# Optimization experiments

Measured on AMD Instinct MI355X. Metric: run time of the kernel, lower is better.

Reference implementation:

```python
import jax, jax.numpy as jnp
import numpy as np

N_HEADS = 16

def setup_inputs() -> dict:
    key = jax.random.key(0)
    ks = jax.random.split(key, 5)
    D = 1024
    B, T = 4, 1024
    scale = 1.0 / np.sqrt(D)
    x = jax.random.normal(ks[0], (B, T, D), dtype=jnp.float32)
    Wq = jax.random.normal(ks[1], (D, D), dtype=jnp.float32) * scale
    Wk = jax.random.normal(ks[2], (D, D), dtype=jnp.float32) * scale
    Wv = jax.random.normal(ks[3], (D, D), dtype=jnp.float32) * scale
    Wo = jax.random.normal(ks[4], (D, D), dtype=jnp.float32) * scale
    return {"x": x, "Wq": Wq, "Wk": Wk, "Wv": Wv, "Wo": Wo}


def reference(x, Wq, Wk, Wv, Wo):
    # FLA BasedLinearAttention (mode='chunk', normalize=True, scale=1) with
    # Taylor feature map phi(u) = [1, u/d^{1/4}, (u (x) u)/sqrt(2 d)], so
    # phi(q)·phi(k) = 1 + s + s^2/2 where s = (q·k)/sqrt(d).
    B, T, D = x.shape
    H = N_HEADS
    d = D // H  # head_dim == feature_dim
    # torch Linear: y = x @ W.T (bias=False in FLA proj layers)
    q = (x @ Wq.T).reshape(B, T, H, d).transpose(0, 2, 1, 3)  # b h t d
    k = (x @ Wk.T).reshape(B, T, H, d).transpose(0, 2, 1, 3)
    v = (x @ Wv.T).reshape(B, T, H, d).transpose(0, 2, 1, 3)
    s = jnp.einsum('bhtd,bhsd->bhts', q, k) / jnp.sqrt(jnp.float32(d))
    scores = 1.0 + s + 0.5 * s * s  # always > 0 (= ((s+1)^2+1)/2)
    causal = jnp.tril(jnp.ones((T, T), dtype=bool))
    scores = jnp.where(causal, scores, 0.0)
    num = jnp.einsum('bhts,bhsd->bhtd', scores, v)
    den = jnp.sum(scores, axis=-1, keepdims=True)
    o = num / den  # b h t d
    o = o.transpose(0, 2, 1, 3).reshape(B, T, D)  # b t (h d)
    return o @ Wo.T
```

## Files before the change

### kernel.cpp

```cpp
#include <hip/hip_runtime.h>

typedef unsigned short u16;
typedef __attribute__((ext_vector_type(8))) short bf16x8;
typedef __attribute__((ext_vector_type(8))) unsigned short u16x8;
typedef __attribute__((ext_vector_type(4))) float f32x4;

#define MFMA16(a, b, c) __builtin_amdgcn_mfma_f32_16x16x32_bf16((a), (b), (c), 0, 0, 0)

__device__ __forceinline__ void gll16(const void* g, void* l) {
    __builtin_amdgcn_global_load_lds(
        (const __attribute__((address_space(1))) unsigned int*)g,
        (__attribute__((address_space(3))) unsigned int*)l, 16, 0, 0);
}

__device__ __forceinline__ u16 f2b(float f) {
    unsigned int u = __float_as_uint(f);
    u += 0x7fffu + ((u >> 16) & 1u);
    return (u16)(u >> 16);
}

__device__ __forceinline__ unsigned int pkcvt(float a, float b) {
    unsigned int r;
    asm("v_cvt_pk_bf16_f32 %0, %1, %2" : "=v"(r) : "v"(a), "v"(b));
    return r;
}

__global__ __launch_bounds__(256) void cast_all(const float* __restrict__ x,
                                                const float* __restrict__ w0,
                                                const float* __restrict__ w1,
                                                const float* __restrict__ w2,
                                                const float* __restrict__ w3,
                                                u16* __restrict__ xb,
                                                u16* __restrict__ wb) {
    const int bid = blockIdx.x;
    const float* s; u16* d; int off;
    if (bid < 2048) { s = x; d = xb; off = bid; }
    else {
        const int wi = (bid - 2048) >> 9;
        s = (wi == 0) ? w0 : (wi == 1) ? w1 : (wi == 2) ? w2 : w3;
        d = wb + (size_t)wi * 1048576;
        off = (bid - 2048) & 511;
    }
    const int i = (off * 256 + threadIdx.x) * 8;
    float4 a = *(const float4*)(s + i);
    float4 b = *(const float4*)(s + i + 4);
    *(uint4*)(d + i) = make_uint4(pkcvt(a.x, a.y), pkcvt(a.z, a.w),
                                  pkcvt(b.x, b.y), pkcvt(b.z, b.w));
}

template <int BM, int BN, int MODE, int SLOTS>
__global__ __launch_bounds__(256) void gemm_bt(const u16* __restrict__ A,
                                               const u16* __restrict__ W,
                                               void* __restrict__ Yv,
                                               u16* __restrict__ vT,
                                               int K, int ldY) {
    constexpr int MI = BM / 32, NJ = BN / 32;
    constexpr int ACH = BM / 16;
    constexpr int NPW = (BM + BN) / 64;
    __shared__ u16 As[2][SLOTS][BM * 32];
    __shared__ u16 Bs[2][SLOTS][BN * 32];
    const int t = threadIdx.x, w = t >> 6, lane = t & 63;
    const int quad = lane >> 4, m16 = lane & 15;
    const int wr = (w >> 1) * (BM / 2), wc = (w & 1) * (BN / 2);
    const int row0 = blockIdx.x * BM, col0 = blockIdx.y * BN;
    const int srow = lane >> 2, scol = (lane & 3) * 8;

    auto stage = [&](int buf, int slot, int k0) {
#pragma unroll
        for (int cc = 0; cc < NPW; ++cc) {
            const int c = w * NPW + cc;
            if (c < ACH)
                gll16(A + (size_t)(row0 + c * 16 + srow) * K + k0 + scol,
                      &As[buf][slot][c * 512]);
            else
                gll16(W + (size_t)(col0 + (c - ACH) * 16 + srow) * K + k0 + scol,
                      &Bs[buf][slot][(c - ACH) * 512]);
        }
    };

    f32x4 acc[MI][NJ];
#pragma unroll
    for (int i = 0; i < MI; ++i)
#pragma unroll
        for (int j = 0; j < NJ; ++j) acc[i][j] = (f32x4){0.f, 0.f, 0.f, 0.f};

    auto compute_tile = [&](int buf, int slot) {
        bf16x8 af[MI], bf[NJ];
#pragma unroll
        for (int i = 0; i < MI; ++i)
            af[i] = *(const bf16x8*)&As[buf][slot][(wr + i * 16 + m16) * 32 + quad * 8];
#pragma unroll
        for (int j = 0; j < NJ; ++j)
            bf[j] = *(const bf16x8*)&Bs[buf][slot][(wc + j * 16 + m16) * 32 + quad * 8];
#pragma unroll
        for (int i = 0; i < MI; ++i)
#pragma unroll
            for (int j = 0; j < NJ; ++j) acc[i][j] = MFMA16(af[i], bf[j], acc[i][j]);
    };

#pragma unroll
    for (int s = 0; s < SLOTS; ++s) stage(0, s, s * 32);
    const int ngroups = K / (32 * SLOTS);
    for (int g = 0; g < ngroups; ++g) {
        const int buf = g & 1;
        __syncthreads();
        const int kn = (g + 1) * SLOTS * 32;
        if (kn < K) {
#pragma unroll
            for (int s = 0; s < SLOTS; ++s) stage(buf ^ 1, s, kn + s * 32);
        }
#pragma unroll
        for (int s = 0; s < SLOTS; ++s) compute_tile(buf, s);
    }
    if constexpr (MODE == 0) {
#pragma unroll
        for (int i = 0; i < MI; ++i)
#pragma unroll
            for (int j = 0; j < NJ; ++j)
#pragma unroll
                for (int r = 0; r < 4; ++r)
                    ((float*)Yv)[(size_t)(row0 + wr + i * 16 + quad * 4 + r) * ldY +
                                 col0 + wc + j * 16 + m16] = acc[i][j][r];
    } else {
        if (col0 < 2048) {
            u16* qk = (u16*)Yv;
#pragma unroll
            for (int i = 0; i < MI; ++i)
#pragma unroll
                for (int j = 0; j < NJ; ++j)
#pragma unroll
                    for (int r = 0; r < 4; ++r)
                        qk[(size_t)(row0 + wr + i * 16 + quad * 4 + r) * 2048 +
                           col0 + wc + j * 16 + m16] = f2b(acc[i][j][r]);
        } else {
#pragma unroll
            for (int i = 0; i < MI; ++i) {
                const int rbase = row0 + wr + i * 16;
                const int bb = rbase >> 10;
                const int tok0 = (rbase & 1023) + quad * 4;
#pragma unroll
                for (int j = 0; j < NJ; ++j) {
                    const int vTrow = bb * 1024 + (col0 + wc + j * 16 + m16 - 2048);
                    *(uint2*)(vT + (size_t)vTrow * 1024 + tok0) =
                        make_uint2(pkcvt(acc[i][j][0], acc[i][j][1]),
                                   pkcvt(acc[i][j][2], acc[i][j][3]));
                }
            }
        }
    }
}

__global__ __launch_bounds__(256) void based_attn(const u16* __restrict__ qkm,
                                                  const u16* __restrict__ vT,
                                                  u16* __restrict__ o) {
    __shared__ u16 ks[2][2][2][64][32];
    __shared__ u16 vs[2][2][2][64][32];
    __shared__ u16 SsA[2][64][32];
    __shared__ u16 SsB[2][64][32];

    const int t = threadIdx.x, w = t >> 6, lane = t & 63;
    const int quad = lane >> 4, m16 = lane & 15;
    const int p = blockIdx.x, h = blockIdx.y, b = blockIdx.z;
    const int tA = p, tB = 15 - p;
    const int srow = lane >> 2, s8 = (lane & 3) * 8;
    const int qrow = w * 16 + m16;

    const size_t qbase = (size_t)b * 1024 * 2048 + h * 64;
    const size_t kbase = qbase + 1024;
    const size_t vbase = ((size_t)b * 1024 + h * 64) * 1024;

    bf16x8 qfA[2], qfB[2];
#pragma unroll
    for (int kd = 0; kd < 2; ++kd) {
        qfA[kd] = *(const bf16x8*)(qkm + qbase +
                   (size_t)(tA * 64 + qrow) * 2048 + kd * 32 + quad * 8);
        qfB[kd] = *(const bf16x8*)(qkm + qbase +
                   (size_t)(tB * 64 + qrow) * 2048 + kd * 32 + quad * 8);
    }

    auto stage_tile = [&](int kt, int buf, int slot) {
#pragma unroll
        for (int cc = 0; cc < 2; ++cc) {
            const int c = w * 2 + cc;
            const int blk = c >> 2, rc = c & 3;
            gll16(qkm + kbase + (size_t)(kt * 64 + rc * 16 + srow) * 2048 + blk * 32 + s8,
                  &ks[buf][slot][blk][rc * 16][0]);
            gll16(vT + vbase + (size_t)(rc * 16 + srow) * 1024 + kt * 64 + blk * 32 + s8,
                  &vs[buf][slot][blk][rc * 16][0]);
        }
    };

    bf16x8 ones;
#pragma unroll
    for (int e = 0; e < 8; ++e) ones[e] = (short)0x3F80;

    f32x4 numA[4], numB[4], denA, denB;
    denA = denB = (f32x4){0.f, 0.f, 0.f, 0.f};
#pragma unroll
    for (int j = 0; j < 4; ++j) numA[j] = numB[j] = (f32x4){0.f, 0.f, 0.f, 0.f};

    auto compute = [&](int buf, int slot, int kt) {
        const bool doA = (kt <= tA);
        f32x4 sA[4], sB[4];
#pragma unroll
        for (int jk = 0; jk < 4; ++jk)
            sA[jk] = sB[jk] = (f32x4){0.f, 0.f, 0.f, 0.f};
        __builtin_amdgcn_s_setprio(1);
#pragma unroll
        for (int kd = 0; kd < 2; ++kd)
#pragma unroll
            for (int jk = 0; jk < 4; ++jk) {
                bf16x8 af = *(const bf16x8*)&ks[buf][slot][kd][jk * 16 + m16][quad * 8];
                sB[jk] = MFMA16(af, qfB[kd], sB[jk]);
                if (doA) sA[jk] = MFMA16(af, qfA[kd], sA[jk]);
            }
        __builtin_amdgcn_s_setprio(0);
#pragma unroll
        for (int jk = 0; jk < 4; ++jk) {
            const int kl = jk * 16 + quad * 4;
            float scB[4];
#pragma unroll
            for (int r = 0; r < 4; ++r) {
                const float u = fmaf(sB[jk][r], 0.125f, 1.0f);
                scB[r] = fmaf(u * 0.5f, u, 0.5f);
            }
            if (kt == tB) {
#pragma unroll
                for (int r = 0; r < 4; ++r)
                    if (kl + r > qrow) scB[r] = 0.f;
            }
            *(uint2*)&SsB[kl >> 5][qrow][kl & 31] =
                make_uint2(pkcvt(scB[0], scB[1]), pkcvt(scB[2], scB[3]));
            if (doA) {
                float scA[4];
#pragma unroll
                for (int r = 0; r < 4; ++r) {
                    const float u = fmaf(sA[jk][r], 0.125f, 1.0f);
                    scA[r] = fmaf(u * 0.5f, u, 0.5f);
                }
                if (kt == tA) {
#pragma unroll
                    for (int r = 0; r < 4; ++r)
                        if (kl + r > qrow) scA[r] = 0.f;
                }
                *(uint2*)&SsA[kl >> 5][qrow][kl & 31] =
                    make_uint2(pkcvt(scA[0], scA[1]), pkcvt(scA[2], scA[3]));
            }
        }
        __builtin_amdgcn_s_setprio(1);
#pragma unroll
        for (int kb = 0; kb < 2; ++kb) {
            bf16x8 vf[4];
#pragma unroll
            for (int j = 0; j < 4; ++j)
                vf[j] = *(const bf16x8*)&vs[buf][slot][kb][j * 16 + m16][quad * 8];
            bf16x8 sfB = *(const bf16x8*)&SsB[kb][qrow][quad * 8];
#pragma unroll
            for (int j = 0; j < 4; ++j) numB[j] = MFMA16(sfB, vf[j], numB[j]);
            denB = MFMA16(sfB, ones, denB);
            if (doA) {
                bf16x8 sfA = *(const bf16x8*)&SsA[kb][qrow][quad * 8];
#pragma unroll
                for (int j = 0; j < 4; ++j) numA[j] = MFMA16(sfA, vf[j], numA[j]);
                denA = MFMA16(sfA, ones, denA);
            }
        }
        __builtin_amdgcn_s_setprio(0);
    };

    stage_tile(0, 0, 0);
    stage_tile(1, 0, 1);

    const int ngroups = (tB + 2) >> 1;
    for (int g = 0; g < ngroups; ++g) {
        const int buf = g & 1;
        __syncthreads();
        const int kn = (g + 1) * 2;
        if (kn <= tB) {
            stage_tile(kn, buf ^ 1, 0);
            if (kn + 1 <= tB) stage_tile(kn + 1, buf ^ 1, 1);
        }
        const int kt0 = g * 2;
        compute(buf, 0, kt0);
        if (kt0 + 1 <= tB) compute(buf, 1, kt0 + 1);
    }

#pragma unroll
    for (int r = 0; r < 4; ++r) {
        const float invA = 1.0f / denA[r], invB = 1.0f / denB[r];
        const int rowoff = w * 16 + quad * 4 + r;
        const size_t tokA = (size_t)(b * 1024 + tA * 64 + rowoff);
        const size_t tokB = (size_t)(b * 1024 + tB * 64 + rowoff);
#pragma unroll
        for (int j = 0; j < 4; ++j) {
            o[tokA * 1024 + h * 64 + j * 16 + m16] = f2b(numA[j][r] * invA);
            o[tokB * 1024 + h * 64 + j * 16 + m16] = f2b(numB[j][r] * invB);
        }
    }
}

extern "C" void kernel_launch(void* const* d_in, const int* in_sizes, int n_in,
                              void* d_out, int out_size, void* d_ws, size_t ws_size,
                              hipStream_t stream) {
    const float* x  = (const float*)d_in[0];
    const float* Wq = (const float*)d_in[1];
    const float* Wk = (const float*)d_in[2];
    const float* Wv = (const float*)d_in[3];
    const float* Wo = (const float*)d_in[4];
    float* out = (float*)d_out;

    const size_t MEL = 4096ull * 1024ull;
    u16* xb   = (u16*)d_ws;
    u16* Wqkv = xb + MEL;
    u16* Wob  = Wqkv + 3ull * 1024 * 1024;
    u16* qk   = Wob + 1024ull * 1024;
    u16* vT   = qk + 2ull * MEL;
    u16* o    = vT + MEL;

    cast_all<<<4096, 256, 0, stream>>>(x, Wq, Wk, Wv, Wo, xb, Wqkv);

    dim3 gq(32, 24);
    gemm_bt<128, 128, 1, 1><<<gq, 256, 0, stream>>>(xb, Wqkv, qk, vT, 1024, 2048);

    dim3 ga(8, 16, 4);
    based_attn<<<ga, 256, 0, stream>>>(qk, vT, o);

    dim3 go(32, 16);
    gemm_bt<128, 64, 0, 2><<<go, 256, 0, stream>>>(o, Wob, (void*)out, nullptr, 1024, 1024);
}
```

Baseline: 160.7 us.

## Use triple-buffered LDS pipeline with explicit vmcnt waits in GEMMs

Replaces the double-buffered GEMM K-loop with a three-stage ring of LDS buffers, keeping two tiles of global_load_lds in flight. Explicit s_waitcnt vmcnt counts plus raw s_barrier calls replace __syncthreads, so each step waits only for the oldest tile. The aim is to hide global load latency better in both the QKV and output projections. In exchange it uses more LDS, which can lower occupancy, and the hand-tuned wait counts are fragile.

```diff
diff --git a/kernel.cpp b/kernel.cpp
--- a/kernel.cpp
+++ b/kernel.cpp
@@ -2,7 +2,6 @@
 
 typedef unsigned short u16;
 typedef __attribute__((ext_vector_type(8))) short bf16x8;
-typedef __attribute__((ext_vector_type(8))) unsigned short u16x8;
 typedef __attribute__((ext_vector_type(4))) float f32x4;
 
 #define MFMA16(a, b, c) __builtin_amdgcn_mfma_f32_16x16x32_bf16((a), (b), (c), 0, 0, 0)
@@ -24,6 +23,13 @@
     asm("v_cvt_pk_bf16_f32 %0, %1, %2" : "=v"(r) : "v"(a), "v"(b));
     return r;
 }
+
+template <int N> __device__ __forceinline__ void waitv();
+template <> __device__ __forceinline__ void waitv<0>() { asm volatile("s_waitcnt vmcnt(0)" ::: "memory"); }
+template <> __device__ __forceinline__ void waitv<3>() { asm volatile("s_waitcnt vmcnt(3)" ::: "memory"); }
+template <> __device__ __forceinline__ void waitv<4>() { asm volatile("s_waitcnt vmcnt(4)" ::: "memory"); }
+template <> __device__ __forceinline__ void waitv<6>() { asm volatile("s_waitcnt vmcnt(6)" ::: "memory"); }
+template <> __device__ __forceinline__ void waitv<8>() { asm volatile("s_waitcnt vmcnt(8)" ::: "memory"); }
 
 __global__ __launch_bounds__(256) void cast_all(const float* __restrict__ x,
                                                 const float* __restrict__ w0,
@@ -48,33 +54,33 @@
                                   pkcvt(b.x, b.y), pkcvt(b.z, b.w));
 }
 
-template <int BM, int BN, int MODE, int SLOTS>
-__global__ __launch_bounds__(256) void gemm_bt(const u16* __restrict__ A,
-                                               const u16* __restrict__ W,
-                                               void* __restrict__ Yv,
-                                               u16* __restrict__ vT,
-                                               int K, int ldY) {
+template <int BM, int BN, int MODE>
+__global__ __launch_bounds__(256) void gemm_bt3(const u16* __restrict__ A,
+                                                const u16* __restrict__ W,
+                                                void* __restrict__ Yv,
+                                                u16* __restrict__ vT,
+                                                int K, int ldY) {
     constexpr int MI = BM / 32, NJ = BN / 32;
     constexpr int ACH = BM / 16;
     constexpr int NPW = (BM + BN) / 64;
-    __shared__ u16 As[2][SLOTS][BM * 32];
-    __shared__ u16 Bs[2][SLOTS][BN * 32];
+    __shared__ u16 As[3][BM * 32];
+    __shared__ u16 Bs[3][BN * 32];
     const int t = threadIdx.x, w = t >> 6, lane = t & 63;
     const int quad = lane >> 4, m16 = lane & 15;
     const int wr = (w >> 1) * (BM / 2), wc = (w & 1) * (BN / 2);
     const int row0 = blockIdx.x * BM, col0 = blockIdx.y * BN;
     const int srow = lane >> 2, scol = (lane & 3) * 8;
 
-    auto stage = [&](int buf, int slot, int k0) {
+    auto stage = [&](int buf, int k0) {
 #pragma unroll
         for (int cc = 0; cc < NPW; ++cc) {
             const int c = w * NPW + cc;
             if (c < ACH)
                 gll16(A + (size_t)(row0 + c * 16 + srow) * K + k0 + scol,
-                      &As[buf][slot][c * 512]);
+                      &As[buf][c * 512]);
             else
                 gll16(W + (size_t)(col0 + (c - ACH) * 16 + srow) * K + k0 + scol,
-                      &Bs[buf][slot][(c - ACH) * 512]);
+                      &Bs[buf][(c - ACH) * 512]);
         }
     };
 
@@ -84,34 +90,36 @@
 #pragma unroll
         for (int j = 0; j < NJ; ++j) acc[i][j] = (f32x4){0.f, 0.f, 0.f, 0.f};
 
-    auto compute_tile = [&](int buf, int slot) {
+    auto compute_tile = [&](int buf) {
         bf16x8 af[MI], bf[NJ];
 #pragma unroll
         for (int i = 0; i < MI; ++i)
-            af[i] = *(const bf16x8*)&As[buf][slot][(wr + i * 16 + m16) * 32 + quad * 8];
+            af[i] = *(const bf16x8*)&As[buf][(wr + i * 16 + m16) * 32 + quad * 8];
 #pragma unroll
         for (int j = 0; j < NJ; ++j)
-            bf[j] = *(const bf16x8*)&Bs[buf][slot][(wc + j * 16 + m16) * 32 + quad * 8];
+            bf[j] = *(const bf16x8*)&Bs[buf][(wc + j * 16 + m16) * 32 + quad * 8];
 #pragma unroll
         for (int i = 0; i < MI; ++i)
 #pragma unroll
             for (int j = 0; j < NJ; ++j) acc[i][j] = MFMA16(af[i], bf[j], acc[i][j]);
     };
 
-#pragma unroll
-    for (int s = 0; s < SLOTS; ++s) stage(0, s, s * 32);
-    const int ngroups = K / (32 * SLOTS);
-    for (int g = 0; g < ngroups; ++g) {
-        const int buf = g & 1;
-        __syncthreads();
-        const int kn = (g + 1) * SLOTS * 32;
-        if (kn < K) {
-#pragma unroll
-            for (int s = 0; s < SLOTS; ++s) stage(buf ^ 1, s, kn + s * 32);
-        }
-#pragma unroll
-        for (int s = 0; s < SLOTS; ++s) compute_tile(buf, s);
-    }
+    const int NKT = K / 32;
+    stage(0, 0); stage(1, 32); stage(2, 64);
+    int buf = 0;
+    for (int kt = 0; kt < NKT; ++kt) {
+        if (kt < NKT - 2)      waitv<2 * NPW>();
+        else if (kt == NKT - 2) waitv<NPW>();
+        else                    waitv<0>();
+        __builtin_amdgcn_s_barrier();
+        __builtin_amdgcn_sched_barrier(0);
+        compute_tile(buf);
+        __builtin_amdgcn_s_barrier();
+        const int kn = (kt + 3) * 32;
+        if (kn < K) stage(buf, kn);
+        buf = (buf == 2) ? 0 : buf + 1;
+    }
+
     if constexpr (MODE == 0) {
 #pragma unroll
         for (int i = 0; i < MI; ++i)
@@ -320,11 +328,11 @@
     cast_all<<<4096, 256, 0, stream>>>(x, Wq, Wk, Wv, Wo, xb, Wqkv);
 
     dim3 gq(32, 24);
-    gemm_bt<128, 128, 1, 1><<<gq, 256, 0, stream>>>(xb, Wqkv, qk, vT, 1024, 2048);
+    gemm_bt3<128, 128, 1><<<gq, 256, 0, stream>>>(xb, Wqkv, qk, vT, 1024, 2048);
 
     dim3 ga(8, 16, 4);
     based_attn<<<ga, 256, 0, stream>>>(qk, vT, o);
 
     dim3 go(32, 16);
-    gemm_bt<128, 64, 0, 2><<<go, 256, 0, stream>>>(o, Wob, (void*)out, nullptr, 1024, 1024);
-}
+    gemm_bt3<128, 64, 0><<<go, 256, 0, stream>>>(o, Wob, (void*)out, nullptr, 1024, 1024);
+}
```

After: 168.8 us. +5.0%, slower.

## Keep attention scores in registers and use 16x16x16 MFMA for PV

Applied to the files above, without the earlier changes.

Drops the LDS round-trip for the score tiles by packing the bf16 scores straight into registers. The PV product is recast as a transposed 16x16x16 bf16 MFMA, so the score accumulator layout serves directly as the B operand. The denominator is now a scalar sum plus cross-lane shuffles instead of an extra MFMA against a ones vector, and the output is written as packed uint2 stores. The cost is twice as many MFMA instructions of half the K depth, plus extra uncoalesced 8-byte LDS reads of V.

```diff
diff --git a/kernel.cpp b/kernel.cpp
--- a/kernel.cpp
+++ b/kernel.cpp
@@ -2,10 +2,20 @@
 
 typedef unsigned short u16;
 typedef __attribute__((ext_vector_type(8))) short bf16x8;
-typedef __attribute__((ext_vector_type(8))) unsigned short u16x8;
+typedef __attribute__((ext_vector_type(4))) short s16x4;
+typedef __attribute__((ext_vector_type(2))) int i32x2;
 typedef __attribute__((ext_vector_type(4))) float f32x4;
 
 #define MFMA16(a, b, c) __builtin_amdgcn_mfma_f32_16x16x32_bf16((a), (b), (c), 0, 0, 0)
+
+__device__ __forceinline__ void mfma161616(i32x2 a, i32x2 b, f32x4& c) {
+#if __has_builtin(__builtin_amdgcn_mfma_f32_16x16x16bf16_1k)
+    union { i32x2 i; s16x4 s; } ua{a}, ub{b};
+    c = __builtin_amdgcn_mfma_f32_16x16x16bf16_1k(ua.s, ub.s, c, 0, 0, 0);
+#else
+    asm("v_mfma_f32_16x16x16_bf16 %0, %1, %2, %0" : "+v"(c) : "v"(a), "v"(b));
+#endif
+}
 
 __device__ __forceinline__ void gll16(const void* g, void* l) {
     __builtin_amdgcn_global_load_lds(
@@ -155,8 +165,6 @@
                                                   u16* __restrict__ o) {
     __shared__ u16 ks[2][2][2][64][32];
     __shared__ u16 vs[2][2][2][64][32];
-    __shared__ u16 SsA[2][64][32];
-    __shared__ u16 SsB[2][64][32];
 
     const int t = threadIdx.x, w = t >> 6, lane = t & 63;
     const int quad = lane >> 4, m16 = lane & 15;
@@ -190,12 +198,8 @@
         }
     };
 
-    bf16x8 ones;
-#pragma unroll
-    for (int e = 0; e < 8; ++e) ones[e] = (short)0x3F80;
-
-    f32x4 numA[4], numB[4], denA, denB;
-    denA = denB = (f32x4){0.f, 0.f, 0.f, 0.f};
+    f32x4 numA[4], numB[4];
+    float densA = 0.f, densB = 0.f;
 #pragma unroll
     for (int j = 0; j < 4; ++j) numA[j] = numB[j] = (f32x4){0.f, 0.f, 0.f, 0.f};
 
@@ -215,6 +219,7 @@
                 if (doA) sA[jk] = MFMA16(af, qfA[kd], sA[jk]);
             }
         __builtin_amdgcn_s_setprio(0);
+        i32x2 sbA[4], sbB[4];
 #pragma unroll
         for (int jk = 0; jk < 4; ++jk) {
             const int kl = jk * 16 + quad * 4;
@@ -229,8 +234,9 @@
                 for (int r = 0; r < 4; ++r)
                     if (kl + r > qrow) scB[r] = 0.f;
             }
-            *(uint2*)&SsB[kl >> 5][qrow][kl & 31] =
-                make_uint2(pkcvt(scB[0], scB[1]), pkcvt(scB[2], scB[3]));
+            densB += scB[0] + scB[1] + scB[2] + scB[3];
+            sbB[jk][0] = (int)pkcvt(scB[0], scB[1]);
+            sbB[jk][1] = (int)pkcvt(scB[2], scB[3]);
             if (doA) {
                 float scA[4];
 #pragma unroll
@@ -243,26 +249,20 @@
                     for (int r = 0; r < 4; ++r)
                         if (kl + r > qrow) scA[r] = 0.f;
                 }
-                *(uint2*)&SsA[kl >> 5][qrow][kl & 31] =
-                    make_uint2(pkcvt(scA[0], scA[1]), pkcvt(scA[2], scA[3]));
+                densA += scA[0] + scA[1] + scA[2] + scA[3];
+                sbA[jk][0] = (int)pkcvt(scA[0], scA[1]);
+                sbA[jk][1] = (int)pkcvt(scA[2], scA[3]);
             }
         }
         __builtin_amdgcn_s_setprio(1);
 #pragma unroll
-        for (int kb = 0; kb < 2; ++kb) {
-            bf16x8 vf[4];
-#pragma unroll
-            for (int j = 0; j < 4; ++j)
-                vf[j] = *(const bf16x8*)&vs[buf][slot][kb][j * 16 + m16][quad * 8];
-            bf16x8 sfB = *(const bf16x8*)&SsB[kb][qrow][quad * 8];
-#pragma unroll
-            for (int j = 0; j < 4; ++j) numB[j] = MFMA16(sfB, vf[j], numB[j]);
-            denB = MFMA16(sfB, ones, denB);
-            if (doA) {
-                bf16x8 sfA = *(const bf16x8*)&SsA[kb][qrow][quad * 8];
-#pragma unroll
-                for (int j = 0; j < 4; ++j) numA[j] = MFMA16(sfA, vf[j], numA[j]);
-                denA = MFMA16(sfA, ones, denA);
+        for (int jk = 0; jk < 4; ++jk) {
+            const int kb = jk >> 1, ko = (jk & 1) * 16 + quad * 4;
+#pragma unroll
+            for (int j = 0; j < 4; ++j) {
+                i32x2 va = *(const i32x2*)&vs[buf][slot][kb][j * 16 + m16][ko];
+                mfma161616(va, sbB[jk], numB[j]);
+                if (doA) mfma161616(va, sbA[jk], numA[j]);
             }
         }
         __builtin_amdgcn_s_setprio(0);
@@ -285,17 +285,19 @@
         if (kt0 + 1 <= tB) compute(buf, 1, kt0 + 1);
     }
 
-#pragma unroll
-    for (int r = 0; r < 4; ++r) {
-        const float invA = 1.0f / denA[r], invB = 1.0f / denB[r];
-        const int rowoff = w * 16 + quad * 4 + r;
-        const size_t tokA = (size_t)(b * 1024 + tA * 64 + rowoff);
-        const size_t tokB = (size_t)(b * 1024 + tB * 64 + rowoff);
-#pragma unroll
-        for (int j = 0; j < 4; ++j) {
-            o[tokA * 1024 + h * 64 + j * 16 + m16] = f2b(numA[j][r] * invA);
-            o[tokB * 1024 + h * 64 + j * 16 + m16] = f2b(numB[j][r] * invB);
-        }
+    densA += __shfl_xor(densA, 16); densA += __shfl_xor(densA, 32);
+    densB += __shfl_xor(densB, 16); densB += __shfl_xor(densB, 32);
+    const float invA = 1.0f / densA, invB = 1.0f / densB;
+    const size_t tokA = (size_t)(b * 1024 + tA * 64 + qrow);
+    const size_t tokB = (size_t)(b * 1024 + tB * 64 + qrow);
+#pragma unroll
+    for (int j = 0; j < 4; ++j) {
+        *(uint2*)(o + tokA * 1024 + h * 64 + j * 16 + quad * 4) =
+            make_uint2(pkcvt(numA[j][0] * invA, numA[j][1] * invA),
+                       pkcvt(numA[j][2] * invA, numA[j][3] * invA));
+        *(uint2*)(o + tokB * 1024 + h * 64 + j * 16 + quad * 4) =
+            make_uint2(pkcvt(numB[j][0] * invB, numB[j][1] * invB),
+                       pkcvt(numB[j][2] * invB, numB[j][3] * invB));
     }
 }
 
```

Result: no change. 163.3 us (+1.6%).
